# Performance work log

Hardware: AMD Instinct MI355X
Metric: run time of the kernel (lower is better)

The kernel has to match this reference:

```python
import jax, jax.numpy as jnp
import numpy as np
from jax import lax

T, B, I, N, C, L = 512, 256, 64, 512, 10, 3
TAU = 2.0  # train_tau=False -> constant, non-trainable


def setup_inputs() -> dict:
    key = jax.random.key(0)
    ks = jax.random.split(key, 12)
    f32 = jnp.float32
    data = jax.random.normal(ks[0], (T, B, I), f32)
    h0 = 0.1 * jax.random.uniform(ks[1], (L, B, N), f32)  # matches 0.1*torch.rand init
    # Linear params; weights stored as [in, out] so y = x @ W + b
    Win = jax.random.normal(ks[2], (I, N), f32) / np.float32(np.sqrt(I))
    b_in = 0.01 * jax.random.normal(ks[3], (N,), f32)
    Whh = jax.random.normal(ks[4], (L, N, N), f32) / np.float32(np.sqrt(N))
    b_hh = 0.01 * jax.random.normal(ks[5], (L, N), f32)
    Whi = jax.random.normal(ks[6], (L - 1, N, N), f32) / np.float32(np.sqrt(N))
    b_hi = 0.01 * jax.random.normal(ks[7], (L - 1, N), f32)
    Wfc = jax.random.normal(ks[8], (N, C), f32) / np.float32(np.sqrt(N))
    b_fc = 0.01 * jax.random.normal(ks[9], (C,), f32)
    return {"data": data, "h0": h0, "Win": Win, "b_in": b_in,
            "Whh": Whh, "b_hh": b_hh, "Whi": Whi, "b_hi": b_hi,
            "Wfc": Wfc, "b_fc": b_fc}


def reference(data, h0, Win, b_in, Whh, b_hh, Whi, b_hi, Wfc, b_fc):
    alpha = 1.0 - 1.0 / TAU
    # forward() zeroes the recurrent diagonal every call
    Whh = Whh * (1.0 - jnp.eye(N, dtype=Whh.dtype))
    x = data @ Win + b_in  # [T, B, N] input projection (single input layer, mean over 1)

    def step(hs, inp):
        h0_, h1_, h2_ = hs
        # layer 0: leaky integration + LeakyReLU; same inp fed to every layer
        n0 = jax.nn.leaky_relu(alpha * h0_ + (h0_ @ Whh[0] + b_hh[0] + inp) / TAU)
        # layer 1 sees the *updated* layer-0 state (sequential within a timestep)
        n1 = jax.nn.leaky_relu(
            alpha * h1_ + (h1_ @ Whh[1] + b_hh[1] + n0 @ Whi[0] + b_hi[0] + inp) / TAU)
        n2 = jax.nn.leaky_relu(
            alpha * h2_ + (h2_ @ Whh[2] + b_hh[2] + n1 @ Whi[1] + b_hi[1] + inp) / TAU)
        return (n0, n1, n2), None

    hs_final, _ = lax.scan(step, (h0[0], h0[1], h0[2]), x)
    out = hs_final[-1] @ Wfc + b_fc  # [B, C], single readout head
    return out
```

## Files before the change

kernel.cpp:

```cpp
#include <hip/hip_runtime.h>
#include <stdint.h>


#define TS    512
#define BB    256
#define NN    512
#define MR    16
#define NRG   16
#define NCT   4
#define RD    8

#define SW(r, c) (((r) << 9) + ((((c) ^ ((r) & 7))) << 3))

typedef __attribute__((ext_vector_type(8))) short s8v;
typedef __attribute__((ext_vector_type(4))) float f4v;
typedef __attribute__((ext_vector_type(4))) unsigned int u4v;

#define MFMA16(a, b, c) __builtin_amdgcn_mfma_f32_16x16x32_bf16((a), (b), (c), 0, 0, 0)

__device__ __forceinline__ short f2bf(float f) {
  union { float f; unsigned u; } v; v.f = f;
  unsigned u = v.u;
  u += 0x7fffu + ((u >> 16) & 1u);
  return (short)(u >> 16);
}

__device__ __forceinline__ s8v pack8(f4v a, f4v b) {
  s8v v;
  v[0] = f2bf(a[0]); v[1] = f2bf(a[1]); v[2] = f2bf(a[2]); v[3] = f2bf(a[3]);
  v[4] = f2bf(b[0]); v[5] = f2bf(b[1]); v[6] = f2bf(b[2]); v[7] = f2bf(b[3]);
  return v;
}

__device__ __forceinline__ void waitvm0() {
  asm volatile("s_waitcnt vmcnt(0)" ::: "memory");
}

__device__ __forceinline__ void stg_sc1_b32(unsigned short* p, unsigned v) {
  asm volatile("global_store_dword %0, %1, off sc1" :: "v"(p), "v"(v) : "memory");
}
__device__ __forceinline__ unsigned agent_ld(const unsigned* p) {
  return __hip_atomic_load(p, __ATOMIC_RELAXED, __HIP_MEMORY_SCOPE_AGENT);
}
__device__ __forceinline__ void agent_st(unsigned* p, unsigned v) {
  __hip_atomic_store(p, v, __ATOMIC_RELAXED, __HIP_MEMORY_SCOPE_AGENT);
}

__device__ __forceinline__ void ld8_sync(u4v o[8],
    unsigned v0, unsigned v1, unsigned v2, unsigned v3,
    const unsigned short* sq, const unsigned short* sp) {
  asm volatile(
      "global_load_dwordx4 %0, %8, %12 sc1\n\t"
      "global_load_dwordx4 %1, %9, %12 sc1\n\t"
      "global_load_dwordx4 %2, %10, %12 sc1\n\t"
      "global_load_dwordx4 %3, %11, %12 sc1\n\t"
      "global_load_dwordx4 %4, %8, %13 sc1\n\t"
      "global_load_dwordx4 %5, %9, %13 sc1\n\t"
      "global_load_dwordx4 %6, %10, %13 sc1\n\t"
      "global_load_dwordx4 %7, %11, %13 sc1\n\t"
      "s_waitcnt vmcnt(0)"
      : "=&v"(o[0]), "=&v"(o[1]), "=&v"(o[2]), "=&v"(o[3]),
        "=&v"(o[4]), "=&v"(o[5]), "=&v"(o[6]), "=&v"(o[7])
      : "v"(v0), "v"(v1), "v"(v2), "v"(v3), "s"(sq), "s"(sp)
      : "memory");
}
__device__ __forceinline__ void ld4_sync(u4v o[4],
    unsigned v0, unsigned v1, unsigned v2, unsigned v3,
    const unsigned short* sb) {
  asm volatile(
      "global_load_dwordx4 %0, %4, %8 sc1\n\t"
      "global_load_dwordx4 %1, %5, %8 sc1\n\t"
      "global_load_dwordx4 %2, %6, %8 sc1\n\t"
      "global_load_dwordx4 %3, %7, %8 sc1\n\t"
      "s_waitcnt vmcnt(0)"
      : "=&v"(o[0]), "=&v"(o[1]), "=&v"(o[2]), "=&v"(o[3])
      : "v"(v0), "v"(v1), "v"(v2), "v"(v3), "s"(sb)
      : "memory");
}

__global__ __launch_bounds__(256, 1) void rnn_pipe(
    const float* __restrict__ data, const float* __restrict__ h0,
    const float* __restrict__ Win,  const float* __restrict__ b_in,
    const float* __restrict__ Whh,  const float* __restrict__ b_hh,
    const float* __restrict__ Whi,  const float* __restrict__ b_hi,
    unsigned short* __restrict__ ring, unsigned* __restrict__ cnt,
    float* __restrict__ hfinal)
{
  __shared__ __attribute__((aligned(16))) unsigned short qtile[MR * NN];
  __shared__ __attribute__((aligned(16))) unsigned short ptile[MR * NN];

  const int bi   = blockIdx.x;
  const int x8   = bi & 7;
  const int rr   = bi >> 3;
  const int half = (rr >= 12) ? 1 : 0;
  const int m    = rr - half * 12;
  const int rg   = x8 * 2 + half;
  const int lay  = m >> 2;
  const int ct   = m & 3;
  const int tid  = threadIdx.x;
  const int wv   = tid >> 6;
  const int lane = tid & 63;
  const int lo   = lane & 15;
  const int q4   = lane >> 4;
  const int row0 = rg * MR;
  const int cw   = ct * 128 + wv * 32;

  const int sidx = (lay * NRG + rg) * NCT + ct;
  unsigned* selfprod = cnt + (size_t)sidx * 32;
  unsigned* selfdone = cnt + (size_t)(256 + sidx) * 32;

  unsigned* pollptr = selfprod;
  int polltype = 0;
  if (lane < 4) {
    pollptr = cnt + (size_t)((lay * NRG + rg) * NCT + lane) * 32;  polltype = 1;
  } else if (lane >= 4 && lane < 8 && lay > 0) {
    pollptr = cnt + (size_t)(((lay - 1) * NRG + rg) * NCT + (lane - 4)) * 32;  polltype = 2;
  } else if (lane >= 8 && lane < 12 && lay < 2) {
    pollptr = cnt + (size_t)(256 + ((lay + 1) * NRG + rg) * NCT + (lane - 8)) * 32;  polltype = 3;
  }

  s8v WH[16][2];
  s8v WI[16][2];
  s8v WX[2][2];
  float biasv[2];
  f4v  hst[2];

  {
    const float* WmH = Whh + (size_t)lay * NN * NN;
    #pragma unroll
    for (int kk = 0; kk < 16; ++kk) {
      #pragma unroll
      for (int nf = 0; nf < 2; ++nf) {
        const int col = cw + nf * 16 + lo;
        s8v v;
        #pragma unroll
        for (int j = 0; j < 8; ++j) {
          const int k = kk * 32 + q4 * 8 + j;
          float f = WmH[(size_t)k * NN + col];
          if (k == col) f = 0.f;
          v[j] = f2bf(f);
        }
        WH[kk][nf] = v;
      }
    }
    if (lay > 0) {
      const float* WmI = Whi + (size_t)(lay - 1) * NN * NN;
      #pragma unroll
      for (int kk = 0; kk < 16; ++kk) {
        #pragma unroll
        for (int nf = 0; nf < 2; ++nf) {
          const int col = cw + nf * 16 + lo;
          s8v v;
          #pragma unroll
          for (int j = 0; j < 8; ++j)
            v[j] = f2bf(WmI[(size_t)(kk * 32 + q4 * 8 + j) * NN + col]);
          WI[kk][nf] = v;
        }
      }
    }
    #pragma unroll
    for (int kk = 0; kk < 2; ++kk) {
      #pragma unroll
      for (int nf = 0; nf < 2; ++nf) {
        const int col = cw + nf * 16 + lo;
        s8v v;
        #pragma unroll
        for (int j = 0; j < 8; ++j)
          v[j] = f2bf(Win[(size_t)(kk * 32 + q4 * 8 + j) * NN + col]);
        WX[kk][nf] = v;
      }
    }
    #pragma unroll
    for (int nf = 0; nf < 2; ++nf) {
      const int col = cw + nf * 16 + lo;
      float b = b_hh[lay * NN + col] + b_in[col];
      if (lay > 0) b += b_hi[(lay - 1) * NN + col];
      biasv[nf] = b;
      #pragma unroll
      for (int r = 0; r < 4; ++r)
        hst[nf][r] = h0[(size_t)lay * BB * NN + (size_t)(row0 + q4 * 4 + r) * NN + col];
    }
  }

  const size_t myring = (size_t)(lay * NRG + rg) * RD;
  const size_t upring = (size_t)((lay - 1) * NRG + rg) * RD;

  unsigned voff0 = (unsigned)((0 * 256 + tid) * 16);
  unsigned voff1 = (unsigned)((1 * 256 + tid) * 16);
  unsigned voff2 = (unsigned)((2 * 256 + tid) * 16);
  unsigned voff3 = (unsigned)((3 * 256 + tid) * 16);

  f4v xa0, xa1, xa2, xa3;
  {
    const float* dsrc = data + ((size_t)0 * BB + row0 + lo) * 64 + q4 * 8;
    xa0 = *(const f4v*)(dsrc + 0);
    xa1 = *(const f4v*)(dsrc + 4);
    xa2 = *(const f4v*)(dsrc + 32);
    xa3 = *(const f4v*)(dsrc + 36);
  }

  for (int t = 0; t < TS; ++t) {
    f4v zero4 = {0.f, 0.f, 0.f, 0.f};
    f4v accQ[2] = {zero4, zero4};
    f4v accP[2] = {zero4, zero4};
    {
      s8v xv0 = pack8(xa0, xa1);
      s8v xv1 = pack8(xa2, xa3);
      accQ[0] = MFMA16(xv0, WX[0][0], accQ[0]);
      accQ[1] = MFMA16(xv0, WX[0][1], accQ[1]);
      accQ[0] = MFMA16(xv1, WX[1][0], accQ[0]);
      accQ[1] = MFMA16(xv1, WX[1][1], accQ[1]);
    }

    unsigned tgt = 0;
    if (polltype == 1) tgt = (unsigned)t;
    else if (polltype == 2) tgt = (unsigned)(t + 1);
    else if (polltype == 3 && t >= RD) tgt = (unsigned)(t - RD + 1);
    for (;;) {
      unsigned v = agent_ld(pollptr);
      if (__all((int)(v >= tgt))) break;
    }

    {
      const unsigned short* qsrc = ring + (myring + ((t - 1) & (RD - 1))) * (MR * NN);
      const unsigned short* psrc = ring + (upring + (t & (RD - 1))) * (MR * NN);
      u4v st[8];
      if (t >= 1 && lay > 0) {
        ld8_sync(st, voff0, voff1, voff2, voff3, qsrc, psrc);
        #pragma unroll
        for (int i = 0; i < 4; ++i) {
          const int g = i * 256 + tid;
          const int r = g >> 6, c = g & 63;
          *(u4v*)(qtile + SW(r, c)) = st[i];
          *(u4v*)(ptile + SW(r, c)) = st[4 + i];
        }
      } else if (t >= 1) {
        ld4_sync(st, voff0, voff1, voff2, voff3, qsrc);
        #pragma unroll
        for (int i = 0; i < 4; ++i) {
          const int g = i * 256 + tid;
          const int r = g >> 6, c = g & 63;
          *(u4v*)(qtile + SW(r, c)) = st[i];
        }
      } else if (lay > 0) {
        ld4_sync(st, voff0, voff1, voff2, voff3, psrc);
        #pragma unroll
        for (int i = 0; i < 4; ++i) {
          const int g = i * 256 + tid;
          const int r = g >> 6, c = g & 63;
          *(u4v*)(ptile + SW(r, c)) = st[i];
        }
      }
    }
    __syncthreads();
    if (tid == 0 && lay > 0)
      agent_st(selfdone, (unsigned)(t + 1));

    if (lay > 0) {
      #pragma unroll
      for (int kk = 0; kk < 16; ++kk) {
        s8v av = *(const s8v*)(ptile + SW(lo, kk * 4 + q4));
        accP[0] = MFMA16(av, WI[kk][0], accP[0]);
        accP[1] = MFMA16(av, WI[kk][1], accP[1]);
      }
    }
    if (t == 0) {
      const float* hsrc = h0 + (size_t)lay * BB * NN + (size_t)(row0 + lo) * NN + q4 * 8;
      #pragma unroll
      for (int kk = 0; kk < 16; ++kk) {
        f4v a = *(const f4v*)(hsrc + kk * 32);
        f4v b = *(const f4v*)(hsrc + kk * 32 + 4);
        s8v av = pack8(a, b);
        accQ[0] = MFMA16(av, WH[kk][0], accQ[0]);
        accQ[1] = MFMA16(av, WH[kk][1], accQ[1]);
      }
    } else {
      #pragma unroll
      for (int kk = 0; kk < 16; ++kk) {
        s8v av = *(const s8v*)(qtile + SW(lo, kk * 4 + q4));
        accQ[0] = MFMA16(av, WH[kk][0], accQ[0]);
        accQ[1] = MFMA16(av, WH[kk][1], accQ[1]);
      }
    }

    {
      unsigned short* rslot = ring + (myring + (t & (RD - 1))) * (MR * NN);
      const int elo = lo & ~1;
      #pragma unroll
      for (int nf = 0; nf < 2; ++nf) {
        #pragma unroll
        for (int r = 0; r < 4; ++r) {
          const int row = q4 * 4 + r;
          float v = 0.5f * hst[nf][r] + 0.5f * (accQ[nf][r] + accP[nf][r] + biasv[nf]);
          v = (v >= 0.f) ? v : 0.01f * v;
          hst[nf][r] = v;
          if (lay == 2 && t == TS - 1)
            hfinal[(size_t)(row0 + row) * NN + (cw + nf * 16 + lo)] = v;
          unsigned b  = (unsigned)(unsigned short)f2bf(v);
          unsigned ob = (unsigned)__shfl_xor((int)b, 1);
          unsigned word = (lo & 1) ? (ob | (b << 16)) : (b | (ob << 16));
          if ((lo & 1) == nf)
            stg_sc1_b32(rslot + (size_t)row * NN + (cw + nf * 16 + elo), word);
        }
      }
    }

    {
      const int tn = (t + 1 < TS) ? t + 1 : t;
      const float* dsrc = data + ((size_t)tn * BB + row0 + lo) * 64 + q4 * 8;
      xa0 = *(const f4v*)(dsrc + 0);
      xa1 = *(const f4v*)(dsrc + 4);
      xa2 = *(const f4v*)(dsrc + 32);
      xa3 = *(const f4v*)(dsrc + 36);
    }
    waitvm0();
    __syncthreads();
    if (tid == 0)
      agent_st(selfprod, (unsigned)(t + 1));
  }
}

__global__ void readout_k(const float* __restrict__ hfinal, const float* __restrict__ Wfc,
                          const float* __restrict__ b_fc, float* __restrict__ out)
{
  const int row = blockIdx.x;
  const int lane = threadIdx.x;
  float a[10];
  #pragma unroll
  for (int c = 0; c < 10; ++c) a[c] = 0.f;
  for (int k = lane; k < NN; k += 64) {
    const float h = hfinal[(size_t)row * NN + k];
    const float* w = Wfc + (size_t)k * 10;
    #pragma unroll
    for (int c = 0; c < 10; ++c) a[c] += h * w[c];
  }
  #pragma unroll
  for (int off = 32; off > 0; off >>= 1) {
    #pragma unroll
    for (int c = 0; c < 10; ++c) a[c] += __shfl_down(a[c], off);
  }
  if (lane == 0) {
    #pragma unroll
    for (int c = 0; c < 10; ++c) out[row * 10 + c] = a[c] + b_fc[c];
  }
}

extern "C" void kernel_launch(void* const* d_in, const int* in_sizes, int n_in,
                              void* d_out, int out_size, void* d_ws, size_t ws_size,
                              hipStream_t stream) {
  (void)in_sizes; (void)n_in; (void)out_size; (void)ws_size;
  const float* data = (const float*)d_in[0];
  const float* h0   = (const float*)d_in[1];
  const float* Win  = (const float*)d_in[2];
  const float* b_in = (const float*)d_in[3];
  const float* Whh  = (const float*)d_in[4];
  const float* b_hh = (const float*)d_in[5];
  const float* Whi  = (const float*)d_in[6];
  const float* b_hi = (const float*)d_in[7];
  const float* Wfc  = (const float*)d_in[8];
  const float* b_fc = (const float*)d_in[9];

  unsigned short* ring = (unsigned short*)d_ws;
  const size_t ring_bytes = (size_t)3 * NRG * RD * MR * NN * 2;
  unsigned* cnt = (unsigned*)((char*)d_ws + ring_bytes);
  float* hfinal = (float*)((char*)d_ws + ring_bytes + 65536);

  hipMemsetAsync(cnt, 0, 65536, stream);
  hipLaunchKernelGGL(rnn_pipe, dim3(192), dim3(256), 0, stream,
                     data, h0, Win, b_in, Whh, b_hh, Whi, b_hi, ring, cnt, hfinal);
  hipLaunchKernelGGL(readout_k, dim3(256), dim3(64), 0, stream,
                     hfinal, Wfc, b_fc, (float*)d_out);
}
```

Baseline: 2.270 ms.

## Pack flags into shared cache lines, poll from one wave with sleep

Result: no change. 2.262 ms (-0.3%).

```diff
diff --git a/kernel.cpp b/kernel.cpp
--- a/kernel.cpp
+++ b/kernel.cpp
@@ -36,8 +36,8 @@
   asm volatile("s_waitcnt vmcnt(0)" ::: "memory");
 }
 
-__device__ __forceinline__ void stg_sc1_b32(unsigned short* p, unsigned v) {
-  asm volatile("global_store_dword %0, %1, off sc1" :: "v"(p), "v"(v) : "memory");
+__device__ __forceinline__ void stg_sc1_b16(unsigned short* p, unsigned v) {
+  asm volatile("global_store_short %0, %1, off sc1" :: "v"(p), "v"(v) : "memory");
 }
 __device__ __forceinline__ unsigned agent_ld(const unsigned* p) {
   return __hip_atomic_load(p, __ATOMIC_RELAXED, __HIP_MEMORY_SCOPE_AGENT);
@@ -105,18 +105,19 @@
   const int row0 = rg * MR;
   const int cw   = ct * 128 + wv * 32;
 
-  const int sidx = (lay * NRG + rg) * NCT + ct;
-  unsigned* selfprod = cnt + (size_t)sidx * 32;
-  unsigned* selfdone = cnt + (size_t)(256 + sidx) * 32;
-
-  unsigned* pollptr = selfprod;
+  unsigned* prodline = cnt + (size_t)(lay * NRG + rg) * 32;
+  unsigned* doneline = cnt + (size_t)(64 + lay * NRG + rg) * 32;
+
+  unsigned* pollptr = cnt;
   int polltype = 0;
-  if (lane < 4) {
-    pollptr = cnt + (size_t)((lay * NRG + rg) * NCT + lane) * 32;  polltype = 1;
-  } else if (lane >= 4 && lane < 8 && lay > 0) {
-    pollptr = cnt + (size_t)(((lay - 1) * NRG + rg) * NCT + (lane - 4)) * 32;  polltype = 2;
-  } else if (lane >= 8 && lane < 12 && lay < 2) {
-    pollptr = cnt + (size_t)(256 + ((lay + 1) * NRG + rg) * NCT + (lane - 8)) * 32;  polltype = 3;
+  if (wv == 0) {
+    if (lane < 4) {
+      pollptr = cnt + (size_t)(lay * NRG + rg) * 32 + lane;                polltype = 1;
+    } else if (lane >= 4 && lane < 8 && lay > 0) {
+      pollptr = cnt + (size_t)((lay - 1) * NRG + rg) * 32 + (lane - 4);    polltype = 2;
+    } else if (lane >= 8 && lane < 12 && lay < 2) {
+      pollptr = cnt + (size_t)(64 + (lay + 1) * NRG + rg) * 32 + (lane - 8); polltype = 3;
+    }
   }
 
   s8v WH[16][2];
@@ -212,14 +213,19 @@
       accQ[1] = MFMA16(xv1, WX[1][1], accQ[1]);
     }
 
-    unsigned tgt = 0;
-    if (polltype == 1) tgt = (unsigned)t;
-    else if (polltype == 2) tgt = (unsigned)(t + 1);
-    else if (polltype == 3 && t >= RD) tgt = (unsigned)(t - RD + 1);
-    for (;;) {
-      unsigned v = agent_ld(pollptr);
-      if (__all((int)(v >= tgt))) break;
-    }
+    if (wv == 0) {
+      unsigned tgt = 0;
+      if (polltype == 1) tgt = (unsigned)t;
+      else if (polltype == 2) tgt = (unsigned)(t + 1);
+      else if (polltype == 3 && t >= RD) tgt = (unsigned)(t - RD + 1);
+      unsigned v = tgt;
+      if (polltype) v = agent_ld(pollptr);
+      while (!__all((int)(v >= tgt))) {
+        asm volatile("s_sleep 1" ::: "memory");
+        if (polltype) v = agent_ld(pollptr);
+      }
+    }
+    __syncthreads();
 
     {
       const unsigned short* qsrc = ring + (myring + ((t - 1) & (RD - 1))) * (MR * NN);
@@ -254,7 +260,7 @@
     }
     __syncthreads();
     if (tid == 0 && lay > 0)
-      agent_st(selfdone, (unsigned)(t + 1));
+      agent_st(doneline + ct, (unsigned)(t + 1));
 
     if (lay > 0) {
       #pragma unroll
@@ -285,22 +291,19 @@
 
     {
       unsigned short* rslot = ring + (myring + (t & (RD - 1))) * (MR * NN);
-      const int elo = lo & ~1;
       #pragma unroll
       for (int nf = 0; nf < 2; ++nf) {
+        const int col = cw + nf * 16 + lo;
         #pragma unroll
         for (int r = 0; r < 4; ++r) {
           const int row = q4 * 4 + r;
           float v = 0.5f * hst[nf][r] + 0.5f * (accQ[nf][r] + accP[nf][r] + biasv[nf]);
           v = (v >= 0.f) ? v : 0.01f * v;
           hst[nf][r] = v;
+          stg_sc1_b16(rslot + (size_t)row * NN + col,
+                      (unsigned)(unsigned short)f2bf(v));
           if (lay == 2 && t == TS - 1)
-            hfinal[(size_t)(row0 + row) * NN + (cw + nf * 16 + lo)] = v;
-          unsigned b  = (unsigned)(unsigned short)f2bf(v);
-          unsigned ob = (unsigned)__shfl_xor((int)b, 1);
-          unsigned word = (lo & 1) ? (ob | (b << 16)) : (b | (ob << 16));
-          if ((lo & 1) == nf)
-            stg_sc1_b32(rslot + (size_t)row * NN + (cw + nf * 16 + elo), word);
+            hfinal[(size_t)(row0 + row) * NN + col] = v;
         }
       }
     }
@@ -316,7 +319,7 @@
     waitvm0();
     __syncthreads();
     if (tid == 0)
-      agent_st(selfprod, (unsigned)(t + 1));
+      agent_st(prodline + ct, (unsigned)(t + 1));
   }
 }
 
```

## Double waves per block so each wave computes one 16-column tile

Applied to the files above, without the earlier changes.

After: 1.980 ms. 12.8% less time.

```diff
diff --git a/kernel.cpp b/kernel.cpp
--- a/kernel.cpp
+++ b/kernel.cpp
@@ -36,8 +36,8 @@
   asm volatile("s_waitcnt vmcnt(0)" ::: "memory");
 }
 
-__device__ __forceinline__ void stg_sc1_b32(unsigned short* p, unsigned v) {
-  asm volatile("global_store_dword %0, %1, off sc1" :: "v"(p), "v"(v) : "memory");
+__device__ __forceinline__ void stg_sc1_b16(unsigned short* p, unsigned v) {
+  asm volatile("global_store_short %0, %1, off sc1" :: "v"(p), "v"(v) : "memory");
 }
 __device__ __forceinline__ unsigned agent_ld(const unsigned* p) {
   return __hip_atomic_load(p, __ATOMIC_RELAXED, __HIP_MEMORY_SCOPE_AGENT);
@@ -46,39 +46,31 @@
   __hip_atomic_store(p, v, __ATOMIC_RELAXED, __HIP_MEMORY_SCOPE_AGENT);
 }
 
-__device__ __forceinline__ void ld8_sync(u4v o[8],
-    unsigned v0, unsigned v1, unsigned v2, unsigned v3,
+__device__ __forceinline__ void ld4_dual(u4v o[4],
+    unsigned vA, unsigned vB,
     const unsigned short* sq, const unsigned short* sp) {
   asm volatile(
-      "global_load_dwordx4 %0, %8, %12 sc1\n\t"
-      "global_load_dwordx4 %1, %9, %12 sc1\n\t"
-      "global_load_dwordx4 %2, %10, %12 sc1\n\t"
-      "global_load_dwordx4 %3, %11, %12 sc1\n\t"
-      "global_load_dwordx4 %4, %8, %13 sc1\n\t"
-      "global_load_dwordx4 %5, %9, %13 sc1\n\t"
-      "global_load_dwordx4 %6, %10, %13 sc1\n\t"
-      "global_load_dwordx4 %7, %11, %13 sc1\n\t"
-      "s_waitcnt vmcnt(0)"
-      : "=&v"(o[0]), "=&v"(o[1]), "=&v"(o[2]), "=&v"(o[3]),
-        "=&v"(o[4]), "=&v"(o[5]), "=&v"(o[6]), "=&v"(o[7])
-      : "v"(v0), "v"(v1), "v"(v2), "v"(v3), "s"(sq), "s"(sp)
-      : "memory");
-}
-__device__ __forceinline__ void ld4_sync(u4v o[4],
-    unsigned v0, unsigned v1, unsigned v2, unsigned v3,
-    const unsigned short* sb) {
-  asm volatile(
-      "global_load_dwordx4 %0, %4, %8 sc1\n\t"
-      "global_load_dwordx4 %1, %5, %8 sc1\n\t"
-      "global_load_dwordx4 %2, %6, %8 sc1\n\t"
-      "global_load_dwordx4 %3, %7, %8 sc1\n\t"
+      "global_load_dwordx4 %0, %4, %6 sc1\n\t"
+      "global_load_dwordx4 %1, %5, %6 sc1\n\t"
+      "global_load_dwordx4 %2, %4, %7 sc1\n\t"
+      "global_load_dwordx4 %3, %5, %7 sc1\n\t"
       "s_waitcnt vmcnt(0)"
       : "=&v"(o[0]), "=&v"(o[1]), "=&v"(o[2]), "=&v"(o[3])
-      : "v"(v0), "v"(v1), "v"(v2), "v"(v3), "s"(sb)
+      : "v"(vA), "v"(vB), "s"(sq), "s"(sp)
       : "memory");
 }
-
-__global__ __launch_bounds__(256, 1) void rnn_pipe(
+__device__ __forceinline__ void ld2_sync(u4v o[2],
+    unsigned vA, unsigned vB, const unsigned short* sb) {
+  asm volatile(
+      "global_load_dwordx4 %0, %2, %4 sc1\n\t"
+      "global_load_dwordx4 %1, %3, %4 sc1\n\t"
+      "s_waitcnt vmcnt(0)"
+      : "=&v"(o[0]), "=&v"(o[1])
+      : "v"(vA), "v"(vB), "s"(sb)
+      : "memory");
+}
+
+__global__ __launch_bounds__(512, 2) void rnn_pipe(
     const float* __restrict__ data, const float* __restrict__ h0,
     const float* __restrict__ Win,  const float* __restrict__ b_in,
     const float* __restrict__ Whh,  const float* __restrict__ b_hh,
@@ -103,7 +95,7 @@
   const int lo   = lane & 15;
   const int q4   = lane >> 4;
   const int row0 = rg * MR;
-  const int cw   = ct * 128 + wv * 32;
+  const int cw   = ct * 128 + wv * 16;
 
   const int sidx = (lay * NRG + rg) * NCT + ct;
   unsigned* selfprod = cnt + (size_t)sidx * 32;
@@ -119,76 +111,61 @@
     pollptr = cnt + (size_t)(256 + ((lay + 1) * NRG + rg) * NCT + (lane - 8)) * 32;  polltype = 3;
   }
 
-  s8v WH[16][2];
-  s8v WI[16][2];
-  s8v WX[2][2];
-  float biasv[2];
-  f4v  hst[2];
+  s8v WH[16];
+  s8v WI[16];
+  s8v WX[2];
+  float biasv;
+  f4v  hst;
 
   {
     const float* WmH = Whh + (size_t)lay * NN * NN;
+    const int col = cw + lo;
     #pragma unroll
     for (int kk = 0; kk < 16; ++kk) {
-      #pragma unroll
-      for (int nf = 0; nf < 2; ++nf) {
-        const int col = cw + nf * 16 + lo;
-        s8v v;
-        #pragma unroll
-        for (int j = 0; j < 8; ++j) {
-          const int k = kk * 32 + q4 * 8 + j;
-          float f = WmH[(size_t)k * NN + col];
-          if (k == col) f = 0.f;
-          v[j] = f2bf(f);
-        }
-        WH[kk][nf] = v;
-      }
+      s8v v;
+      #pragma unroll
+      for (int j = 0; j < 8; ++j) {
+        const int k = kk * 32 + q4 * 8 + j;
+        float f = WmH[(size_t)k * NN + col];
+        if (k == col) f = 0.f;
+        v[j] = f2bf(f);
+      }
+      WH[kk] = v;
     }
     if (lay > 0) {
       const float* WmI = Whi + (size_t)(lay - 1) * NN * NN;
       #pragma unroll
       for (int kk = 0; kk < 16; ++kk) {
-        #pragma unroll
-        for (int nf = 0; nf < 2; ++nf) {
-          const int col = cw + nf * 16 + lo;
-          s8v v;
-          #pragma unroll
-          for (int j = 0; j < 8; ++j)
-            v[j] = f2bf(WmI[(size_t)(kk * 32 + q4 * 8 + j) * NN + col]);
-          WI[kk][nf] = v;
-        }
-      }
-    }
-    #pragma unroll
-    for (int kk = 0; kk < 2; ++kk) {
-      #pragma unroll
-      for (int nf = 0; nf < 2; ++nf) {
-        const int col = cw + nf * 16 + lo;
         s8v v;
         #pragma unroll
         for (int j = 0; j < 8; ++j)
-          v[j] = f2bf(Win[(size_t)(kk * 32 + q4 * 8 + j) * NN + col]);
-        WX[kk][nf] = v;
-      }
-    }
-    #pragma unroll
-    for (int nf = 0; nf < 2; ++nf) {
-      const int col = cw + nf * 16 + lo;
-      float b = b_hh[lay * NN + col] + b_in[col];
-      if (lay > 0) b += b_hi[(lay - 1) * NN + col];
-      biasv[nf] = b;
-      #pragma unroll
-      for (int r = 0; r < 4; ++r)
-        hst[nf][r] = h0[(size_t)lay * BB * NN + (size_t)(row0 + q4 * 4 + r) * NN + col];
-    }
+          v[j] = f2bf(WmI[(size_t)(kk * 32 + q4 * 8 + j) * NN + col]);
+        WI[kk] = v;
+      }
+    }
+    #pragma unroll
+    for (int kk = 0; kk < 2; ++kk) {
+      s8v v;
+      #pragma unroll
+      for (int j = 0; j < 8; ++j)
+        v[j] = f2bf(Win[(size_t)(kk * 32 + q4 * 8 + j) * NN + col]);
+      WX[kk] = v;
+    }
+    float b = b_hh[lay * NN + col] + b_in[col];
+    if (lay > 0) b += b_hi[(lay - 1) * NN + col];
+    biasv = b;
+    #pragma unroll
+    for (int r = 0; r < 4; ++r)
+      hst[r] = h0[(size_t)lay * BB * NN + (size_t)(row0 + q4 * 4 + r) * NN + col];
   }
 
   const size_t myring = (size_t)(lay * NRG + rg) * RD;
   const size_t upring = (size_t)((lay - 1) * NRG + rg) * RD;
 
-  unsigned voff0 = (unsigned)((0 * 256 + tid) * 16);
-  unsigned voff1 = (unsigned)((1 * 256 + tid) * 16);
-  unsigned voff2 = (unsigned)((2 * 256 + tid) * 16);
-  unsigned voff3 = (unsigned)((3 * 256 + tid) * 16);
+  unsigned voffA = (unsigned)((0 * 512 + tid) * 16);
+  unsigned voffB = (unsigned)((1 * 512 + tid) * 16);
+  const int gA_r = tid >> 6,           gA_c = tid & 63;
+  const int gB_r = (512 + tid) >> 6,   gB_c = tid & 63;
 
   f4v xa0, xa1, xa2, xa3;
   {
@@ -201,15 +178,13 @@
 
   for (int t = 0; t < TS; ++t) {
     f4v zero4 = {0.f, 0.f, 0.f, 0.f};
-    f4v accQ[2] = {zero4, zero4};
-    f4v accP[2] = {zero4, zero4};
+    f4v accQ = zero4;
+    f4v accP = zero4;
     {
       s8v xv0 = pack8(xa0, xa1);
       s8v xv1 = pack8(xa2, xa3);
-      accQ[0] = MFMA16(xv0, WX[0][0], accQ[0]);
-      accQ[1] = MFMA16(xv0, WX[0][1], accQ[1]);
-      accQ[0] = MFMA16(xv1, WX[1][0], accQ[0]);
-      accQ[1] = MFMA16(xv1, WX[1][1], accQ[1]);
+      accQ = MFMA16(xv0, WX[0], accQ);
+      accQ = MFMA16(xv1, WX[1], accQ);
     }
 
     unsigned tgt = 0;
@@ -224,32 +199,23 @@
     {
       const unsigned short* qsrc = ring + (myring + ((t - 1) & (RD - 1))) * (MR * NN);
       const unsigned short* psrc = ring + (upring + (t & (RD - 1))) * (MR * NN);
-      u4v st[8];
       if (t >= 1 && lay > 0) {
-        ld8_sync(st, voff0, voff1, voff2, voff3, qsrc, psrc);
-        #pragma unroll
-        for (int i = 0; i < 4; ++i) {
-          const int g = i * 256 + tid;
-          const int r = g >> 6, c = g & 63;
-          *(u4v*)(qtile + SW(r, c)) = st[i];
-          *(u4v*)(ptile + SW(r, c)) = st[4 + i];
-        }
+        u4v st[4];
+        ld4_dual(st, voffA, voffB, qsrc, psrc);
+        *(u4v*)(qtile + SW(gA_r, gA_c)) = st[0];
+        *(u4v*)(qtile + SW(gB_r, gB_c)) = st[1];
+        *(u4v*)(ptile + SW(gA_r, gA_c)) = st[2];
+        *(u4v*)(ptile + SW(gB_r, gB_c)) = st[3];
       } else if (t >= 1) {
-        ld4_sync(st, voff0, voff1, voff2, voff3, qsrc);
-        #pragma unroll
-        for (int i = 0; i < 4; ++i) {
-          const int g = i * 256 + tid;
-          const int r = g >> 6, c = g & 63;
-          *(u4v*)(qtile + SW(r, c)) = st[i];
-        }
+        u4v st[2];
+        ld2_sync(st, voffA, voffB, qsrc);
+        *(u4v*)(qtile + SW(gA_r, gA_c)) = st[0];
+        *(u4v*)(qtile + SW(gB_r, gB_c)) = st[1];
       } else if (lay > 0) {
-        ld4_sync(st, voff0, voff1, voff2, voff3, psrc);
-        #pragma unroll
-        for (int i = 0; i < 4; ++i) {
-          const int g = i * 256 + tid;
-          const int r = g >> 6, c = g & 63;
-          *(u4v*)(ptile + SW(r, c)) = st[i];
-        }
+        u4v st[2];
+        ld2_sync(st, voffA, voffB, psrc);
+        *(u4v*)(ptile + SW(gA_r, gA_c)) = st[0];
+        *(u4v*)(ptile + SW(gB_r, gB_c)) = st[1];
       }
     }
     __syncthreads();
@@ -260,8 +226,7 @@
       #pragma unroll
       for (int kk = 0; kk < 16; ++kk) {
         s8v av = *(const s8v*)(ptile + SW(lo, kk * 4 + q4));
-        accP[0] = MFMA16(av, WI[kk][0], accP[0]);
-        accP[1] = MFMA16(av, WI[kk][1], accP[1]);
+        accP = MFMA16(av, WI[kk], accP);
       }
     }
     if (t == 0) {
@@ -271,37 +236,29 @@
         f4v a = *(const f4v*)(hsrc + kk * 32);
         f4v b = *(const f4v*)(hsrc + kk * 32 + 4);
         s8v av = pack8(a, b);
-        accQ[0] = MFMA16(av, WH[kk][0], accQ[0]);
-        accQ[1] = MFMA16(av, WH[kk][1], accQ[1]);
+        accQ = MFMA16(av, WH[kk], accQ);
       }
     } else {
       #pragma unroll
       for (int kk = 0; kk < 16; ++kk) {
         s8v av = *(const s8v*)(qtile + SW(lo, kk * 4 + q4));
-        accQ[0] = MFMA16(av, WH[kk][0], accQ[0]);
-        accQ[1] = MFMA16(av, WH[kk][1], accQ[1]);
+        accQ = MFMA16(av, WH[kk], accQ);
       }
     }
 
     {
       unsigned short* rslot = ring + (myring + (t & (RD - 1))) * (MR * NN);
-      const int elo = lo & ~1;
-      #pragma unroll
-      for (int nf = 0; nf < 2; ++nf) {
-        #pragma unroll
-        for (int r = 0; r < 4; ++r) {
-          const int row = q4 * 4 + r;
-          float v = 0.5f * hst[nf][r] + 0.5f * (accQ[nf][r] + accP[nf][r] + biasv[nf]);
-          v = (v >= 0.f) ? v : 0.01f * v;
-          hst[nf][r] = v;
-          if (lay == 2 && t == TS - 1)
-            hfinal[(size_t)(row0 + row) * NN + (cw + nf * 16 + lo)] = v;
-          unsigned b  = (unsigned)(unsigned short)f2bf(v);
-          unsigned ob = (unsigned)__shfl_xor((int)b, 1);
-          unsigned word = (lo & 1) ? (ob | (b << 16)) : (b | (ob << 16));
-          if ((lo & 1) == nf)
-            stg_sc1_b32(rslot + (size_t)row * NN + (cw + nf * 16 + elo), word);
-        }
+      const int col = cw + lo;
+      #pragma unroll
+      for (int r = 0; r < 4; ++r) {
+        const int row = q4 * 4 + r;
+        float v = 0.5f * hst[r] + 0.5f * (accQ[r] + accP[r] + biasv);
+        v = (v >= 0.f) ? v : 0.01f * v;
+        hst[r] = v;
+        stg_sc1_b16(rslot + (size_t)row * NN + col,
+                    (unsigned)(unsigned short)f2bf(v));
+        if (lay == 2 && t == TS - 1)
+          hfinal[(size_t)(row0 + row) * NN + col] = v;
       }
     }
 
@@ -366,7 +323,7 @@
   float* hfinal = (float*)((char*)d_ws + ring_bytes + 65536);
 
   hipMemsetAsync(cnt, 0, 65536, stream);
-  hipLaunchKernelGGL(rnn_pipe, dim3(192), dim3(256), 0, stream,
+  hipLaunchKernelGGL(rnn_pipe, dim3(192), dim3(512), 0, stream,
                      data, h0, Win, b_in, Whh, b_hh, Whi, b_hi, ring, cnt, hfinal);
   hipLaunchKernelGGL(readout_k, dim3(256), dim3(64), 0, stream,
                      hfinal, Wfc, b_fc, (float*)d_out);
```
